# Kernel tuning notes

Hardware: AMD Instinct MI355X
Metric: run time of the kernel (lower is better)

Reference implementation:

```python
import jax, jax.numpy as jnp
import numpy as np

N = 100000
E = 1600000
NFEAT = 128
NHID1 = 128
NHID2 = 128
NCLASS = 40


def setup_inputs() -> dict:
    key = jax.random.key(0)
    ks = jax.random.split(key, 16)
    x = jax.random.normal(ks[0], (N, NFEAT), dtype=jnp.float32)
    src = jax.random.randint(ks[1], (E,), 0, N, dtype=jnp.int32)
    dst = jax.random.randint(ks[2], (E,), 0, N, dtype=jnp.int32)
    s = 0.05
    params = {
        # SAGE layer 1: self branch and neighbor branch
        'w1s': jax.random.normal(ks[3], (NFEAT, NHID1), dtype=jnp.float32) * s,
        'b1s': jnp.zeros((NHID1,), dtype=jnp.float32),
        'w1n': jax.random.normal(ks[4], (NFEAT, NHID1), dtype=jnp.float32) * s,
        'b1n': jnp.zeros((NHID1,), dtype=jnp.float32),
        # SAGE layer 2 (input dim 2*NHID1)
        'w2s': jax.random.normal(ks[5], (2 * NHID1, NHID2), dtype=jnp.float32) * s,
        'b2s': jnp.zeros((NHID2,), dtype=jnp.float32),
        'w2n': jax.random.normal(ks[6], (2 * NHID1, NHID2), dtype=jnp.float32) * s,
        'b2n': jnp.zeros((NHID2,), dtype=jnp.float32),
        # final linear head (input dim 2*NHID2)
        'wfc': jax.random.normal(ks[7], (2 * NHID2, NCLASS), dtype=jnp.float32) * s,
        'bfc': jnp.zeros((NCLASS,), dtype=jnp.float32),
    }
    return {'x': x, 'src': src, 'dst': dst, **params}


def _neigh_mean(h, src, dst, n_nodes):
    # mean aggregation == spmm(row-normalized adj, h), via segment sum over edges
    msg = jax.ops.segment_sum(h[src], dst, num_segments=n_nodes)  # [N, d]
    cnt = jax.ops.segment_sum(jnp.ones((src.shape[0],), h.dtype), dst, num_segments=n_nodes)
    return msg / jnp.maximum(cnt, 1.0)[:, None]


def _sage_layer(h, src, dst, ws, bs, wn, bn):
    neigh = _neigh_mean(h, src, dst, h.shape[0])
    return jnp.concatenate([h @ ws + bs, neigh @ wn + bn], axis=1)


def _l2_normalize(h, eps=1e-12):
    nrm = jnp.sqrt(jnp.sum(h * h, axis=1, keepdims=True))
    return h / jnp.maximum(nrm, eps)


def reference(x, src, dst, w1s, b1s, w1n, b1n, w2s, b2s, w2n, b2n, wfc, bfc):
    h = jax.nn.relu(_sage_layer(x, src, dst, w1s, b1s, w1n, b1n))  # [N, 2*NHID1]
    h = _l2_normalize(h)
    # dropout is identity in eval mode
    h = jax.nn.relu(_sage_layer(h, src, dst, w2s, b2s, w2n, b2n))  # [N, 2*NHID2]
    h = _l2_normalize(h)
    return h @ wfc + bfc  # [N, NCLASS]
```

## Files before the change

### kernel.cpp

```cpp
#include <hip/hip_runtime.h>
#include <hip/hip_bf16.h>


#define N_NODES 100000
#define N_EDGES 1600000
#define NBUCK   196
#define BCAP    12288
#define PB_CAP  14336
#define CHUNK   4096

typedef unsigned short u16;
typedef unsigned int u32;
typedef __bf16 bf16x8 __attribute__((ext_vector_type(8)));
typedef float  f32x4  __attribute__((ext_vector_type(4)));

__device__ __forceinline__ u16 f2b(float f) {
  unsigned x = __builtin_bit_cast(unsigned, f);
  unsigned r = x + 0x7fffu + ((x >> 16) & 1u);
  return (u16)(r >> 16);
}
__device__ __forceinline__ bf16x8 ldfrag(const u16* p) {
  uint4 u = *reinterpret_cast<const uint4*>(p);
  return __builtin_bit_cast(bf16x8, u);
}
__device__ __forceinline__ void unpack8(uint4 u, float* f) {
  f[0] = __builtin_bit_cast(float, u.x << 16);
  f[1] = __builtin_bit_cast(float, u.x & 0xffff0000u);
  f[2] = __builtin_bit_cast(float, u.y << 16);
  f[3] = __builtin_bit_cast(float, u.y & 0xffff0000u);
  f[4] = __builtin_bit_cast(float, u.z << 16);
  f[5] = __builtin_bit_cast(float, u.z & 0xffff0000u);
  f[6] = __builtin_bit_cast(float, u.w << 16);
  f[7] = __builtin_bit_cast(float, u.w & 0xffff0000u);
}
__device__ __forceinline__ uint4 pack8(const float* f) {
  uint4 u;
  u.x = (u32)f2b(f[0]) | ((u32)f2b(f[1]) << 16);
  u.y = (u32)f2b(f[2]) | ((u32)f2b(f[3]) << 16);
  u.z = (u32)f2b(f[4]) | ((u32)f2b(f[5]) << 16);
  u.w = (u32)f2b(f[6]) | ((u32)f2b(f[7]) << 16);
  return u;
}

__global__ __launch_bounds__(256) void prep_weights(
    const float* __restrict__ w1s, const float* __restrict__ w1n,
    const float* __restrict__ w2s, const float* __restrict__ w2n,
    const float* __restrict__ wfc,
    u16* __restrict__ WT1, u16* __restrict__ WT2, u16* __restrict__ WFCT,
    int* __restrict__ cntg, u16* __restrict__ XWn) {
  int i = blockIdx.x * 256 + threadIdx.x;
  if (i < 32768) {
    int c = i >> 7, k = i & 127;
    float v = (c < 128) ? w1s[k * 128 + c] : w1n[k * 128 + (c - 128)];
    WT1[c * 128 + k] = f2b(v);
  } else if (i < 32768 + 65536) {
    int j = i - 32768;
    int c = j >> 8, k = j & 255;
    float v = (c < 128) ? w2s[k * 128 + c] : w2n[k * 128 + (c - 128)];
    WT2[c * 256 + k] = f2b(v);
  } else if (i < 98304 + 12288) {
    int j = i - 98304;
    int c = j >> 8, k = j & 255;
    float v = (c < 40) ? wfc[k * 40 + c] : 0.f;
    WFCT[c * 256 + k] = f2b(v);
  } else {
    int t = threadIdx.x;
    if (t < NBUCK) cntg[t] = 0;
    if (t >= 128 && t < 256) XWn[(size_t)N_NODES * 128 + (t - 128)] = 0;
  }
}

__device__ __forceinline__ int wave_incl_scan(int x, int lane) {
#pragma unroll
  for (int d = 1; d < 64; d <<= 1) {
    int n = __shfl_up(x, d, 64);
    if (lane >= d) x += n;
  }
  return x;
}

__global__ __launch_bounds__(256) void bucket_kernel(
    const int* __restrict__ src, const int* __restrict__ dst,
    int* __restrict__ cntg, u32* __restrict__ pairBuf) {
  __shared__ unsigned hist[NBUCK];
  __shared__ unsigned gbase[NBUCK];
  __shared__ int sws[4];
  __shared__ u32 stage[CHUNK];
  __shared__ int tgt[CHUNK];
  const int tid = threadIdx.x, lane = tid & 63, wid = tid >> 6;
  const int e0 = blockIdx.x * CHUNK;

  for (int i = tid; i < NBUCK; i += 256) hist[i] = 0u;
  __syncthreads();

  u32 myW[16];
  int myR[16], myB[16];
#pragma unroll
  for (int k = 0; k < 16; ++k) {
    int e = e0 + k * 256 + tid;
    if (e < N_EDGES) {
      unsigned d = (unsigned)dst[e];
      myW[k] = ((d & 511u) << 17) | (unsigned)src[e];
      myB[k] = (int)(d >> 9);
      myR[k] = (int)atomicAdd(&hist[myB[k]], 1u);
    } else {
      myB[k] = -1;
    }
  }
  __syncthreads();

  int cnt = (tid < NBUCK) ? (int)hist[tid] : 0;
  int inc = wave_incl_scan(cnt, lane);
  if (lane == 63) sws[wid] = inc;
  __syncthreads();
  if (wid == 0) {
    int s = (lane < 4) ? sws[lane] : 0;
    s = wave_incl_scan(s, lane);
    if (lane < 4) sws[lane] = s;
  }
  __syncthreads();
  int excl = (wid ? sws[wid - 1] : 0) + inc - cnt;
  int gofs = 0;
  if (tid < NBUCK && cnt > 0) gofs = tid * BCAP + atomicAdd(&cntg[tid], cnt);
  __syncthreads();
  if (tid < NBUCK) {
    hist[tid] = (unsigned)excl;
    gbase[tid] = (unsigned)gofs;
  }
  __syncthreads();

#pragma unroll
  for (int k = 0; k < 16; ++k) {
    if (myB[k] >= 0) {
      int slot = (int)hist[myB[k]] + myR[k];
      stage[slot] = myW[k];
      tgt[slot] = (int)gbase[myB[k]] + myR[k];
    }
  }
  __syncthreads();
  int nvalid = N_EDGES - e0;
  if (nvalid > CHUNK) nvalid = CHUNK;
  for (int i = tid; i < nvalid; i += 256) pairBuf[tgt[i]] = stage[i];
}

__global__ __launch_bounds__(512) void csr_build(
    const u32* __restrict__ pairBuf, const int* __restrict__ cntg,
    int* __restrict__ rowptr, int* __restrict__ degA, int* __restrict__ csr) {
  __shared__ int lcnt[512];
  __shared__ int lofs[512];
  __shared__ int sws[8];
  __shared__ int cstage[PB_CAP];
  const int b = blockIdx.x, tid = threadIdx.x;
  const int lane = tid & 63, wid = tid >> 6;
  int nb = cntg[b];
  if (nb > BCAP) nb = BCAP;
  const u32* pp = pairBuf + (size_t)b * BCAP;

  lcnt[tid] = 0;
  __syncthreads();
  for (int i = tid; i < nb; i += 512) atomicAdd(&lcnt[(pp[i] >> 17) & 511], 1);
  __syncthreads();
  int dg = lcnt[tid];
  int pd = (dg + 7) & ~7;
  int inc = wave_incl_scan(pd, lane);
  if (lane == 63) sws[wid] = inc;
  __syncthreads();
  if (wid == 0) {
    int s = (lane < 8) ? sws[lane] : 0;
    s = wave_incl_scan(s, lane);
    if (lane < 8) sws[lane] = s;
  }
  __syncthreads();
  int excl = (wid ? sws[wid - 1] : 0) + inc - pd;
  int ptot = sws[7];
  int node = b * 512 + tid;
  if (node < N_NODES) {
    rowptr[node] = b * PB_CAP + excl;
    degA[node] = dg;
  }
  lofs[tid] = excl;
  __syncthreads();
  for (int i = tid; i < nb; i += 512) {
    u32 pr = pp[i];
    int pos = atomicAdd(&lofs[(pr >> 17) & 511], 1);
    if (pos < PB_CAP) cstage[pos] = (int)(pr & 0x1FFFFu);
  }
  __syncthreads();
  for (int k = excl + dg; k < excl + pd; ++k)
    if (k < PB_CAP) cstage[k] = N_NODES;
  __syncthreads();
  if (ptot > PB_CAP) ptot = PB_CAP;
  for (int i = tid; i < ptot; i += 512) csr[b * PB_CAP + i] = cstage[i];
}

__device__ __forceinline__ void agg_node(
    const u16* __restrict__ Xs, const u16* __restrict__ Xn,
    const int* __restrict__ rowptr, const int* __restrict__ degA,
    const int* __restrict__ csr, const float* __restrict__ bs,
    const float* __restrict__ bn, int node, int g, int lc,
    float* sf, float* nf) {
  int beg = rowptr[node], dg = degA[node];
  int cnt = (dg + 7) & ~7;
  float acc[8] = {0.f, 0.f, 0.f, 0.f, 0.f, 0.f, 0.f, 0.f};
  const u16* colbase = Xn + lc * 8;
  const int* cp = csr + beg;
  for (int j = 0; j < cnt; j += 8) {
    int s0 = cp[j + g];
    int s1 = cp[j + 4 + g];
    uint4 u0 = *reinterpret_cast<const uint4*>(colbase + (size_t)s0 * 128);
    uint4 u1 = *reinterpret_cast<const uint4*>(colbase + (size_t)s1 * 128);
    float f0[8], f1[8];
    unpack8(u0, f0);
    unpack8(u1, f1);
#pragma unroll
    for (int i = 0; i < 8; ++i) acc[i] += f0[i] + f1[i];
  }
#pragma unroll
  for (int i = 0; i < 8; ++i) {
    acc[i] += __shfl_xor(acc[i], 32, 64);
    acc[i] += __shfl_xor(acc[i], 16, 64);
  }
  float inv = 1.f / (float)(dg > 0 ? dg : 1);
  uint4 sv4 = *reinterpret_cast<const uint4*>(Xs + (size_t)node * 128 + lc * 8);
  unpack8(sv4, sf);
  float4 b0 = *reinterpret_cast<const float4*>(bs + lc * 8);
  float4 b1 = *reinterpret_cast<const float4*>(bs + lc * 8 + 4);
  float4 c0 = *reinterpret_cast<const float4*>(bn + lc * 8);
  float4 c1 = *reinterpret_cast<const float4*>(bn + lc * 8 + 4);
  float bsv[8] = {b0.x, b0.y, b0.z, b0.w, b1.x, b1.y, b1.z, b1.w};
  float bnv[8] = {c0.x, c0.y, c0.z, c0.w, c1.x, c1.y, c1.z, c1.w};
  float ss = 0.f;
#pragma unroll
  for (int i = 0; i < 8; ++i) {
    sf[i] = fmaxf(sf[i] + bsv[i], 0.f);
    nf[i] = fmaxf(acc[i] * inv + bnv[i], 0.f);
    ss += sf[i] * sf[i] + nf[i] * nf[i];
  }
  ss += __shfl_xor(ss, 1, 64);
  ss += __shfl_xor(ss, 2, 64);
  ss += __shfl_xor(ss, 4, 64);
  ss += __shfl_xor(ss, 8, 64);
  float sc = 1.f / fmaxf(sqrtf(ss), 1e-12f);
#pragma unroll
  for (int i = 0; i < 8; ++i) {
    sf[i] *= sc;
    nf[i] *= sc;
  }
}

__global__ __launch_bounds__(256) void agg_epi_kernel(
    const u16* __restrict__ Xs, const u16* __restrict__ Xn,
    const int* __restrict__ rowptr, const int* __restrict__ degA,
    const int* __restrict__ csr, const float* __restrict__ bs,
    const float* __restrict__ bn, u16* __restrict__ H) {
  int node = (int)((blockIdx.x * 256 + threadIdx.x) >> 6);
  int lane = threadIdx.x & 63;
  if (node >= N_NODES) return;
  const int g = lane >> 4, lc = lane & 15;
  float sf[8], nf[8];
  agg_node(Xs, Xn, rowptr, degA, csr, bs, bn, node, g, lc, sf, nf);
  if (g == 0) {
    *reinterpret_cast<uint4*>(H + (size_t)node * 256 + lc * 8) = pack8(sf);
  } else if (g == 1) {
    *reinterpret_cast<uint4*>(H + (size_t)node * 256 + 128 + lc * 8) = pack8(nf);
  }
}

__global__ __launch_bounds__(512) void agg_fc_kernel(
    const u16* __restrict__ Xs, const u16* __restrict__ Xn,
    const int* __restrict__ rowptr, const int* __restrict__ degA,
    const int* __restrict__ csr, const float* __restrict__ bs,
    const float* __restrict__ bn, const u16* __restrict__ WFCT,
    const float* __restrict__ bfc, float* __restrict__ Out) {
  __shared__ u16 hh[32][264];
  __shared__ u16 wf[48][264];
  const int tid = threadIdx.x, w = tid >> 6, lane = tid & 63;
  const int g = lane >> 4, lc = lane & 15;
  const int nb0 = blockIdx.x * 32;

  for (int i = tid; i < 1536; i += 512) {
    int row = i >> 5, col = (i & 31) * 8;
    *reinterpret_cast<uint4*>(&wf[row][col]) =
        *reinterpret_cast<const uint4*>(WFCT + row * 256 + col);
  }

  for (int t = 0; t < 4; ++t) {
    int r = w * 4 + t;
    int node = nb0 + r;
    if (node < N_NODES) {
      float sf[8], nf[8];
      agg_node(Xs, Xn, rowptr, degA, csr, bs, bn, node, g, lc, sf, nf);
      if (g == 0) {
        *reinterpret_cast<uint4*>(&hh[r][lc * 8]) = pack8(sf);
      } else if (g == 1) {
        *reinterpret_cast<uint4*>(&hh[r][128 + lc * 8]) = pack8(nf);
      }
    } else {
      uint4 z = {0u, 0u, 0u, 0u};
      if (g == 0) *reinterpret_cast<uint4*>(&hh[r][lc * 8]) = z;
      else if (g == 1) *reinterpret_cast<uint4*>(&hh[r][128 + lc * 8]) = z;
    }
  }
  __syncthreads();

  const int rt = w & 1, cg = w >> 1;
  if (cg < 3) {
    const int lrow = lane & 15, lk = lane >> 4;
    f32x4 acc = {0.f, 0.f, 0.f, 0.f};
#pragma unroll
    for (int ks = 0; ks < 8; ++ks) {
      bf16x8 a = ldfrag(&hh[rt * 16 + lrow][ks * 32 + lk * 8]);
      bf16x8 b = ldfrag(&wf[cg * 16 + lrow][ks * 32 + lk * 8]);
      acc = __builtin_amdgcn_mfma_f32_16x16x32_bf16(a, b, acc, 0, 0, 0);
    }
#pragma unroll
    for (int j = 0; j < 4; ++j) {
      int row = nb0 + rt * 16 + lk * 4 + j;
      int col = cg * 16 + lrow;
      if (row < N_NODES && col < 40) Out[(size_t)row * 40 + col] = acc[j] + bfc[col];
    }
  }
}

__global__ __launch_bounds__(512) void gemm1_kernel(
    const float* __restrict__ A, const u16* __restrict__ WT,
    u16* __restrict__ Cs, u16* __restrict__ Cn) {
  __shared__ u16 lb[256 * 128];
  char* lbc = reinterpret_cast<char*>(lb);
  const int tid = threadIdx.x;
  for (int i = tid; i < 4096; i += 512) {
    uint4 v = *reinterpret_cast<const uint4*>(WT + i * 8);
    int byte = i * 16;
    int swz = byte ^ (((byte >> 8) & 7) << 4);
    *reinterpret_cast<uint4*>(lbc + swz) = v;
  }

  const int w = tid >> 6, lane = tid & 63;
  const int lrow = lane & 15, lk = lane >> 4;
  const int xr = (lrow & 7) << 4;
  const int rbase = blockIdx.x * 128 + w * 16;

  bf16x8 af[4];
  {
    int r = rbase + lrow;
    if (r >= N_NODES) r = N_NODES - 1;
    const float* ap = A + (size_t)r * 128 + lk * 8;
#pragma unroll
    for (int ks = 0; ks < 4; ++ks) {
      float4 f0 = *reinterpret_cast<const float4*>(ap + ks * 32);
      float4 f1 = *reinterpret_cast<const float4*>(ap + ks * 32 + 4);
      float f[8] = {f0.x, f0.y, f0.z, f0.w, f1.x, f1.y, f1.z, f1.w};
      af[ks] = __builtin_bit_cast(bf16x8, pack8(f));
    }
  }
  __syncthreads();

  f32x4 acc[16];
#pragma unroll
  for (int ct = 0; ct < 16; ++ct) acc[ct] = f32x4{0.f, 0.f, 0.f, 0.f};
#pragma unroll
  for (int ks = 0; ks < 4; ++ks) {
#pragma unroll
    for (int ct = 0; ct < 16; ++ct) {
      int byte = (ct * 16 + lrow) * 256 + ks * 64 + lk * 16;
      bf16x8 b = __builtin_bit_cast(
          bf16x8, *reinterpret_cast<const uint4*>(lbc + (byte ^ xr)));
      acc[ct] = __builtin_amdgcn_mfma_f32_16x16x32_bf16(af[ks], b, acc[ct], 0, 0, 0);
    }
  }
#pragma unroll
  for (int j = 0; j < 4; ++j) {
    int r = rbase + lk * 4 + j;
    if (r < N_NODES) {
      u16* cs = Cs + (size_t)r * 128 + lrow;
      u16* cn = Cn + (size_t)r * 128 + lrow;
#pragma unroll
      for (int ct = 0; ct < 8; ++ct) cs[ct * 16] = f2b(acc[ct][j]);
#pragma unroll
      for (int ct = 0; ct < 8; ++ct) cn[ct * 16] = f2b(acc[8 + ct][j]);
    }
  }
}

__global__ __launch_bounds__(512) void gemm2_kernel(
    const u16* __restrict__ A, const u16* __restrict__ WT,
    u16* __restrict__ Cs, u16* __restrict__ Cn) {
  __shared__ u16 lb[128 * 256];
  char* lbc = reinterpret_cast<char*>(lb);
  const int tid = threadIdx.x;
  const int w = tid >> 6, lane = tid & 63;
  const int lrow = lane & 15, lk = lane >> 4;
  const int xr = (lrow & 7) << 4;
  const int rbase = blockIdx.x * 128 + w * 16;

  bf16x8 af[8];
  {
    int r = rbase + lrow;
    if (r >= N_NODES) r = N_NODES - 1;
    const u16* ap = A + (size_t)r * 256 + lk * 8;
#pragma unroll
    for (int ks = 0; ks < 8; ++ks) af[ks] = ldfrag(ap + ks * 32);
  }

#pragma unroll
  for (int half = 0; half < 2; ++half) {
    const u16* Wsrc = WT + (size_t)half * 128 * 256;
    for (int i = tid; i < 4096; i += 512) {
      uint4 v = *reinterpret_cast<const uint4*>(Wsrc + i * 8);
      int byte = i * 16;
      int swz = byte ^ (((byte >> 9) & 7) << 4);
      *reinterpret_cast<uint4*>(lbc + swz) = v;
    }
    __syncthreads();

    f32x4 acc[8];
#pragma unroll
    for (int ct = 0; ct < 8; ++ct) acc[ct] = f32x4{0.f, 0.f, 0.f, 0.f};
#pragma unroll
    for (int ks = 0; ks < 8; ++ks) {
#pragma unroll
      for (int ct = 0; ct < 8; ++ct) {
        int byte = (ct * 16 + lrow) * 512 + ks * 64 + lk * 16;
        bf16x8 b = __builtin_bit_cast(
            bf16x8, *reinterpret_cast<const uint4*>(lbc + (byte ^ xr)));
        acc[ct] = __builtin_amdgcn_mfma_f32_16x16x32_bf16(af[ks], b, acc[ct], 0, 0, 0);
      }
    }
    u16* __restrict__ Cout = half ? Cn : Cs;
#pragma unroll
    for (int j = 0; j < 4; ++j) {
      int r = rbase + lk * 4 + j;
      if (r < N_NODES) {
        u16* cp = Cout + (size_t)r * 128 + lrow;
#pragma unroll
        for (int ct = 0; ct < 8; ++ct) cp[ct * 16] = f2b(acc[ct][j]);
      }
    }
    __syncthreads();
  }
}

extern "C" void kernel_launch(void* const* d_in, const int* in_sizes, int n_in,
                              void* d_out, int out_size, void* d_ws, size_t ws_size,
                              hipStream_t stream) {
  const float* x = (const float*)d_in[0];
  const int* src = (const int*)d_in[1];
  const int* dst = (const int*)d_in[2];
  const float* w1s = (const float*)d_in[3];
  const float* b1s = (const float*)d_in[4];
  const float* w1n = (const float*)d_in[5];
  const float* b1n = (const float*)d_in[6];
  const float* w2s = (const float*)d_in[7];
  const float* b2s = (const float*)d_in[8];
  const float* w2n = (const float*)d_in[9];
  const float* b2n = (const float*)d_in[10];
  const float* wfc = (const float*)d_in[11];
  const float* bfc = (const float*)d_in[12];
  float* out = (float*)d_out;

  char* p = (char*)d_ws;
  auto alloc = [&](size_t bytes) {
    char* r = p;
    p += (bytes + 255) & ~(size_t)255;
    return r;
  };
  u16* XWs = (u16*)alloc((size_t)N_NODES * 128 * 2);
  u16* XWn = (u16*)alloc(((size_t)N_NODES + 1) * 128 * 2);
  u16* h1 = (u16*)alloc((size_t)N_NODES * 256 * 2);
  u16* WT1 = (u16*)alloc(32768 * 2);
  u16* WT2 = (u16*)alloc(65536 * 2);
  u16* WFCT = (u16*)alloc(12288 * 2);
  u32* pairBuf = (u32*)alloc((size_t)NBUCK * BCAP * 4);
  int* cntg = (int*)alloc(NBUCK * 4);
  int* rowptr = (int*)alloc((size_t)N_NODES * 4);
  int* degA = (int*)alloc((size_t)N_NODES * 4);
  int* csr = (int*)alloc((size_t)NBUCK * PB_CAP * 4);

  prep_weights<<<433, 256, 0, stream>>>(w1s, w1n, w2s, w2n, wfc, WT1, WT2, WFCT,
                                        cntg, XWn);
  bucket_kernel<<<391, 256, 0, stream>>>(src, dst, cntg, pairBuf);
  csr_build<<<NBUCK, 512, 0, stream>>>(pairBuf, cntg, rowptr, degA, csr);

  gemm1_kernel<<<782, 512, 0, stream>>>(x, WT1, XWs, XWn);
  agg_epi_kernel<<<25000, 256, 0, stream>>>(XWs, XWn, rowptr, degA, csr, b1s, b1n, h1);
  gemm2_kernel<<<782, 512, 0, stream>>>(h1, WT2, XWs, XWn);
  agg_fc_kernel<<<3125, 512, 0, stream>>>(XWs, XWn, rowptr, degA, csr, b2s, b2n,
                                          WFCT, bfc, out);
}
```

Baseline: 359.9 us.

## Merge setup kernels, co-schedule CSR build with GEMM1, persistent layer-1 aggregation

Weight prep and edge bucketing become one launch, split by block index. CSR construction and the first GEMM share a second launch, split the same way, using 64KB of dynamic shared memory. This cuts kernel launches and lets the two independent stages overlap on the device. The bucket-counter and pad-row zeroing move to hipMemsetAsync calls. The layer-1 aggregation becomes a grid-stride loop over 2048 blocks. The final aggregation+FC kernel now uses an XOR-swizzled LDS tile and reads the FC weights straight from global memory instead of staging them.

```diff
diff --git a/kernel.cpp b/kernel.cpp
--- a/kernel.cpp
+++ b/kernel.cpp
@@ -8,6 +8,8 @@
 #define BCAP    12288
 #define PB_CAP  14336
 #define CHUNK   4096
+#define PREP_BLKS 432
+#define GEMM1_BLKS 782
 
 typedef unsigned short u16;
 typedef unsigned int u32;
@@ -42,13 +44,22 @@
   return u;
 }
 
-__global__ __launch_bounds__(256) void prep_weights(
-    const float* __restrict__ w1s, const float* __restrict__ w1n,
-    const float* __restrict__ w2s, const float* __restrict__ w2n,
-    const float* __restrict__ wfc,
-    u16* __restrict__ WT1, u16* __restrict__ WT2, u16* __restrict__ WFCT,
-    int* __restrict__ cntg, u16* __restrict__ XWn) {
-  int i = blockIdx.x * 256 + threadIdx.x;
+__device__ __forceinline__ int wave_incl_scan(int x, int lane) {
+#pragma unroll
+  for (int d = 1; d < 64; d <<= 1) {
+    int n = __shfl_up(x, d, 64);
+    if (lane >= d) x += n;
+  }
+  return x;
+}
+
+__device__ void prep_body(int bid, const float* __restrict__ w1s,
+                          const float* __restrict__ w1n,
+                          const float* __restrict__ w2s,
+                          const float* __restrict__ w2n,
+                          const float* __restrict__ wfc, u16* __restrict__ WT1,
+                          u16* __restrict__ WT2, u16* __restrict__ WFCT) {
+  int i = bid * 256 + threadIdx.x;
   if (i < 32768) {
     int c = i >> 7, k = i & 127;
     float v = (c < 128) ? w1s[k * 128 + c] : w1n[k * 128 + (c - 128)];
@@ -58,37 +69,32 @@
     int c = j >> 8, k = j & 255;
     float v = (c < 128) ? w2s[k * 128 + c] : w2n[k * 128 + (c - 128)];
     WT2[c * 256 + k] = f2b(v);
-  } else if (i < 98304 + 12288) {
+  } else {
     int j = i - 98304;
     int c = j >> 8, k = j & 255;
     float v = (c < 40) ? wfc[k * 40 + c] : 0.f;
     WFCT[c * 256 + k] = f2b(v);
-  } else {
-    int t = threadIdx.x;
-    if (t < NBUCK) cntg[t] = 0;
-    if (t >= 128 && t < 256) XWn[(size_t)N_NODES * 128 + (t - 128)] = 0;
-  }
-}
-
-__device__ __forceinline__ int wave_incl_scan(int x, int lane) {
-#pragma unroll
-  for (int d = 1; d < 64; d <<= 1) {
-    int n = __shfl_up(x, d, 64);
-    if (lane >= d) x += n;
-  }
-  return x;
-}
-
-__global__ __launch_bounds__(256) void bucket_kernel(
+  }
+}
+
+__global__ __launch_bounds__(256) void prep_bucket_kernel(
+    const float* __restrict__ w1s, const float* __restrict__ w1n,
+    const float* __restrict__ w2s, const float* __restrict__ w2n,
+    const float* __restrict__ wfc, u16* __restrict__ WT1,
+    u16* __restrict__ WT2, u16* __restrict__ WFCT,
     const int* __restrict__ src, const int* __restrict__ dst,
     int* __restrict__ cntg, u32* __restrict__ pairBuf) {
+  if (blockIdx.x < PREP_BLKS) {
+    prep_body(blockIdx.x, w1s, w1n, w2s, w2n, wfc, WT1, WT2, WFCT);
+    return;
+  }
   __shared__ unsigned hist[NBUCK];
   __shared__ unsigned gbase[NBUCK];
   __shared__ int sws[4];
   __shared__ u32 stage[CHUNK];
   __shared__ int tgt[CHUNK];
   const int tid = threadIdx.x, lane = tid & 63, wid = tid >> 6;
-  const int e0 = blockIdx.x * CHUNK;
+  const int e0 = (blockIdx.x - PREP_BLKS) * CHUNK;
 
   for (int i = tid; i < NBUCK; i += 256) hist[i] = 0u;
   __syncthreads();
@@ -143,14 +149,14 @@
   for (int i = tid; i < nvalid; i += 256) pairBuf[tgt[i]] = stage[i];
 }
 
-__global__ __launch_bounds__(512) void csr_build(
-    const u32* __restrict__ pairBuf, const int* __restrict__ cntg,
-    int* __restrict__ rowptr, int* __restrict__ degA, int* __restrict__ csr) {
-  __shared__ int lcnt[512];
-  __shared__ int lofs[512];
-  __shared__ int sws[8];
-  __shared__ int cstage[PB_CAP];
-  const int b = blockIdx.x, tid = threadIdx.x;
+__device__ void csr_body(char* smem, int b, const u32* __restrict__ pairBuf,
+                         const int* __restrict__ cntg, int* __restrict__ rowptr,
+                         int* __restrict__ degA, int* __restrict__ csr) {
+  int* lcnt = (int*)smem;
+  int* lofs = lcnt + 512;
+  int* sws = lofs + 512;
+  int* cstage = sws + 8;
+  const int tid = threadIdx.x;
   const int lane = tid & 63, wid = tid >> 6;
   int nb = cntg[b];
   if (nb > BCAP) nb = BCAP;
@@ -191,6 +197,79 @@
   __syncthreads();
   if (ptot > PB_CAP) ptot = PB_CAP;
   for (int i = tid; i < ptot; i += 512) csr[b * PB_CAP + i] = cstage[i];
+}
+
+__device__ void gemm1_body(char* smem, int bid, const float* __restrict__ A,
+                           const u16* __restrict__ WT, u16* __restrict__ Cs,
+                           u16* __restrict__ Cn) {
+  u16* lb = (u16*)smem;
+  char* lbc = smem;
+  const int tid = threadIdx.x;
+  for (int i = tid; i < 4096; i += 512) {
+    uint4 v = *reinterpret_cast<const uint4*>(WT + i * 8);
+    int byte = i * 16;
+    int swz = byte ^ (((byte >> 8) & 7) << 4);
+    *reinterpret_cast<uint4*>(lbc + swz) = v;
+  }
+
+  const int w = tid >> 6, lane = tid & 63;
+  const int lrow = lane & 15, lk = lane >> 4;
+  const int xr = (lrow & 7) << 4;
+  const int rbase = bid * 128 + w * 16;
+
+  bf16x8 af[4];
+  {
+    int r = rbase + lrow;
+    if (r >= N_NODES) r = N_NODES - 1;
+    const float* ap = A + (size_t)r * 128 + lk * 8;
+#pragma unroll
+    for (int ks = 0; ks < 4; ++ks) {
+      float4 f0 = *reinterpret_cast<const float4*>(ap + ks * 32);
+      float4 f1 = *reinterpret_cast<const float4*>(ap + ks * 32 + 4);
+      float f[8] = {f0.x, f0.y, f0.z, f0.w, f1.x, f1.y, f1.z, f1.w};
+      af[ks] = __builtin_bit_cast(bf16x8, pack8(f));
+    }
+  }
+  __syncthreads();
+
+  f32x4 acc[16];
+#pragma unroll
+  for (int ct = 0; ct < 16; ++ct) acc[ct] = f32x4{0.f, 0.f, 0.f, 0.f};
+#pragma unroll
+  for (int ks = 0; ks < 4; ++ks) {
+#pragma unroll
+    for (int ct = 0; ct < 16; ++ct) {
+      int byte = (ct * 16 + lrow) * 256 + ks * 64 + lk * 16;
+      bf16x8 b = __builtin_bit_cast(
+          bf16x8, *reinterpret_cast<const uint4*>(lbc + (byte ^ xr)));
+      acc[ct] = __builtin_amdgcn_mfma_f32_16x16x32_bf16(af[ks], b, acc[ct], 0, 0, 0);
+    }
+  }
+#pragma unroll
+  for (int j = 0; j < 4; ++j) {
+    int r = rbase + lk * 4 + j;
+    if (r < N_NODES) {
+      u16* cs = Cs + (size_t)r * 128 + lrow;
+      u16* cn = Cn + (size_t)r * 128 + lrow;
+#pragma unroll
+      for (int ct = 0; ct < 8; ++ct) cs[ct * 16] = f2b(acc[ct][j]);
+#pragma unroll
+      for (int ct = 0; ct < 8; ++ct) cn[ct * 16] = f2b(acc[8 + ct][j]);
+    }
+  }
+}
+
+__global__ __launch_bounds__(512) void csr_gemm1_kernel(
+    const u32* __restrict__ pairBuf, const int* __restrict__ cntg,
+    int* __restrict__ rowptr, int* __restrict__ degA, int* __restrict__ csr,
+    const float* __restrict__ A, const u16* __restrict__ WT,
+    u16* __restrict__ Cs, u16* __restrict__ Cn) {
+  extern __shared__ char smem[];
+  if (blockIdx.x < NBUCK) {
+    csr_body(smem, blockIdx.x, pairBuf, cntg, rowptr, degA, csr);
+  } else {
+    gemm1_body(smem, blockIdx.x - NBUCK, A, WT, Cs, Cn);
+  }
 }
 
 __device__ __forceinline__ void agg_node(
@@ -253,131 +332,17 @@
     const int* __restrict__ rowptr, const int* __restrict__ degA,
     const int* __restrict__ csr, const float* __restrict__ bs,
     const float* __restrict__ bn, u16* __restrict__ H) {
-  int node = (int)((blockIdx.x * 256 + threadIdx.x) >> 6);
-  int lane = threadIdx.x & 63;
-  if (node >= N_NODES) return;
+  const int lane = threadIdx.x & 63;
   const int g = lane >> 4, lc = lane & 15;
-  float sf[8], nf[8];
-  agg_node(Xs, Xn, rowptr, degA, csr, bs, bn, node, g, lc, sf, nf);
-  if (g == 0) {
-    *reinterpret_cast<uint4*>(H + (size_t)node * 256 + lc * 8) = pack8(sf);
-  } else if (g == 1) {
-    *reinterpret_cast<uint4*>(H + (size_t)node * 256 + 128 + lc * 8) = pack8(nf);
-  }
-}
-
-__global__ __launch_bounds__(512) void agg_fc_kernel(
-    const u16* __restrict__ Xs, const u16* __restrict__ Xn,
-    const int* __restrict__ rowptr, const int* __restrict__ degA,
-    const int* __restrict__ csr, const float* __restrict__ bs,
-    const float* __restrict__ bn, const u16* __restrict__ WFCT,
-    const float* __restrict__ bfc, float* __restrict__ Out) {
-  __shared__ u16 hh[32][264];
-  __shared__ u16 wf[48][264];
-  const int tid = threadIdx.x, w = tid >> 6, lane = tid & 63;
-  const int g = lane >> 4, lc = lane & 15;
-  const int nb0 = blockIdx.x * 32;
-
-  for (int i = tid; i < 1536; i += 512) {
-    int row = i >> 5, col = (i & 31) * 8;
-    *reinterpret_cast<uint4*>(&wf[row][col]) =
-        *reinterpret_cast<const uint4*>(WFCT + row * 256 + col);
-  }
-
-  for (int t = 0; t < 4; ++t) {
-    int r = w * 4 + t;
-    int node = nb0 + r;
-    if (node < N_NODES) {
-      float sf[8], nf[8];
-      agg_node(Xs, Xn, rowptr, degA, csr, bs, bn, node, g, lc, sf, nf);
-      if (g == 0) {
-        *reinterpret_cast<uint4*>(&hh[r][lc * 8]) = pack8(sf);
-      } else if (g == 1) {
-        *reinterpret_cast<uint4*>(&hh[r][128 + lc * 8]) = pack8(nf);
-      }
-    } else {
-      uint4 z = {0u, 0u, 0u, 0u};
-      if (g == 0) *reinterpret_cast<uint4*>(&hh[r][lc * 8]) = z;
-      else if (g == 1) *reinterpret_cast<uint4*>(&hh[r][128 + lc * 8]) = z;
-    }
-  }
-  __syncthreads();
-
-  const int rt = w & 1, cg = w >> 1;
-  if (cg < 3) {
-    const int lrow = lane & 15, lk = lane >> 4;
-    f32x4 acc = {0.f, 0.f, 0.f, 0.f};
-#pragma unroll
-    for (int ks = 0; ks < 8; ++ks) {
-      bf16x8 a = ldfrag(&hh[rt * 16 + lrow][ks * 32 + lk * 8]);
-      bf16x8 b = ldfrag(&wf[cg * 16 + lrow][ks * 32 + lk * 8]);
-      acc = __builtin_amdgcn_mfma_f32_16x16x32_bf16(a, b, acc, 0, 0, 0);
-    }
-#pragma unroll
-    for (int j = 0; j < 4; ++j) {
-      int row = nb0 + rt * 16 + lk * 4 + j;
-      int col = cg * 16 + lrow;
-      if (row < N_NODES && col < 40) Out[(size_t)row * 40 + col] = acc[j] + bfc[col];
-    }
-  }
-}
-
-__global__ __launch_bounds__(512) void gemm1_kernel(
-    const float* __restrict__ A, const u16* __restrict__ WT,
-    u16* __restrict__ Cs, u16* __restrict__ Cn) {
-  __shared__ u16 lb[256 * 128];
-  char* lbc = reinterpret_cast<char*>(lb);
-  const int tid = threadIdx.x;
-  for (int i = tid; i < 4096; i += 512) {
-    uint4 v = *reinterpret_cast<const uint4*>(WT + i * 8);
-    int byte = i * 16;
-    int swz = byte ^ (((byte >> 8) & 7) << 4);
-    *reinterpret_cast<uint4*>(lbc + swz) = v;
-  }
-
-  const int w = tid >> 6, lane = tid & 63;
-  const int lrow = lane & 15, lk = lane >> 4;
-  const int xr = (lrow & 7) << 4;
-  const int rbase = blockIdx.x * 128 + w * 16;
-
-  bf16x8 af[4];
-  {
-    int r = rbase + lrow;
-    if (r >= N_NODES) r = N_NODES - 1;
-    const float* ap = A + (size_t)r * 128 + lk * 8;
-#pragma unroll
-    for (int ks = 0; ks < 4; ++ks) {
-      float4 f0 = *reinterpret_cast<const float4*>(ap + ks * 32);
-      float4 f1 = *reinterpret_cast<const float4*>(ap + ks * 32 + 4);
-      float f[8] = {f0.x, f0.y, f0.z, f0.w, f1.x, f1.y, f1.z, f1.w};
-      af[ks] = __builtin_bit_cast(bf16x8, pack8(f));
-    }
-  }
-  __syncthreads();
-
-  f32x4 acc[16];
-#pragma unroll
-  for (int ct = 0; ct < 16; ++ct) acc[ct] = f32x4{0.f, 0.f, 0.f, 0.f};
-#pragma unroll
-  for (int ks = 0; ks < 4; ++ks) {
-#pragma unroll
-    for (int ct = 0; ct < 16; ++ct) {
-      int byte = (ct * 16 + lrow) * 256 + ks * 64 + lk * 16;
-      bf16x8 b = __builtin_bit_cast(
-          bf16x8, *reinterpret_cast<const uint4*>(lbc + (byte ^ xr)));
-      acc[ct] = __builtin_amdgcn_mfma_f32_16x16x32_bf16(af[ks], b, acc[ct], 0, 0, 0);
-    }
-  }
-#pragma unroll
-  for (int j = 0; j < 4; ++j) {
-    int r = rbase + lk * 4 + j;
-    if (r < N_NODES) {
-      u16* cs = Cs + (size_t)r * 128 + lrow;
-      u16* cn = Cn + (size_t)r * 128 + lrow;
-#pragma unroll
-      for (int ct = 0; ct < 8; ++ct) cs[ct * 16] = f2b(acc[ct][j]);
-#pragma unroll
-      for (int ct = 0; ct < 8; ++ct) cn[ct * 16] = f2b(acc[8 + ct][j]);
+  const int wave0 = blockIdx.x * 4 + (threadIdx.x >> 6);
+  const int stride = gridDim.x * 4;
+  for (int node = wave0; node < N_NODES; node += stride) {
+    float sf[8], nf[8];
+    agg_node(Xs, Xn, rowptr, degA, csr, bs, bn, node, g, lc, sf, nf);
+    if (g == 0) {
+      *reinterpret_cast<uint4*>(H + (size_t)node * 256 + lc * 8) = pack8(sf);
+    } else if (g == 1) {
+      *reinterpret_cast<uint4*>(H + (size_t)node * 256 + 128 + lc * 8) = pack8(nf);
     }
   }
 }
@@ -437,6 +402,64 @@
       }
     }
     __syncthreads();
+  }
+}
+
+__global__ __launch_bounds__(512) void agg_fc_kernel(
+    const u16* __restrict__ Xs, const u16* __restrict__ Xn,
+    const int* __restrict__ rowptr, const int* __restrict__ degA,
+    const int* __restrict__ csr, const float* __restrict__ bs,
+    const float* __restrict__ bn, const u16* __restrict__ WFCT,
+    const float* __restrict__ bfc, float* __restrict__ Out) {
+  __shared__ u16 hh[32 * 256];
+  char* hhb = reinterpret_cast<char*>(hh);
+  const int tid = threadIdx.x, w = tid >> 6, lane = tid & 63;
+  const int g = lane >> 4, lc = lane & 15;
+  const int nb0 = blockIdx.x * 32;
+
+  for (int t = 0; t < 4; ++t) {
+    int r = w * 4 + t;
+    int node = nb0 + r;
+    int xr_r = (r & 7) << 4;
+    uint4 val;
+    int cbyte;
+    if (node < N_NODES) {
+      float sf[8], nf[8];
+      agg_node(Xs, Xn, rowptr, degA, csr, bs, bn, node, g, lc, sf, nf);
+      val = (g == 0) ? pack8(sf) : pack8(nf);
+    } else {
+      val = uint4{0u, 0u, 0u, 0u};
+    }
+    if (g == 0) {
+      cbyte = (lc * 16) ^ xr_r;
+      *reinterpret_cast<uint4*>(hhb + r * 512 + cbyte) = val;
+    } else if (g == 1) {
+      cbyte = 256 + ((lc * 16) ^ xr_r);
+      *reinterpret_cast<uint4*>(hhb + r * 512 + cbyte) = val;
+    }
+  }
+  __syncthreads();
+
+  const int rt = w & 1, cg = w >> 1;
+  if (cg < 3) {
+    const int lrow = lane & 15, lk = lane >> 4;
+    const int arow = rt * 16 + lrow;
+    const int xr_a = (arow & 7) << 4;
+    f32x4 acc = {0.f, 0.f, 0.f, 0.f};
+#pragma unroll
+    for (int ks = 0; ks < 8; ++ks) {
+      int cbyte = (ks * 64 + lk * 16) ^ xr_a;
+      bf16x8 a = __builtin_bit_cast(
+          bf16x8, *reinterpret_cast<const uint4*>(hhb + arow * 512 + cbyte));
+      bf16x8 b = ldfrag(WFCT + (size_t)(cg * 16 + lrow) * 256 + ks * 32 + lk * 8);
+      acc = __builtin_amdgcn_mfma_f32_16x16x32_bf16(a, b, acc, 0, 0, 0);
+    }
+#pragma unroll
+    for (int j = 0; j < 4; ++j) {
+      int row = nb0 + rt * 16 + lk * 4 + j;
+      int col = cg * 16 + lrow;
+      if (row < N_NODES && col < 40) Out[(size_t)row * 40 + col] = acc[j] + bfc[col];
+    }
   }
 }
 
@@ -476,14 +499,15 @@
   int* degA = (int*)alloc((size_t)N_NODES * 4);
   int* csr = (int*)alloc((size_t)NBUCK * PB_CAP * 4);
 
-  prep_weights<<<433, 256, 0, stream>>>(w1s, w1n, w2s, w2n, wfc, WT1, WT2, WFCT,
-                                        cntg, XWn);
-  bucket_kernel<<<391, 256, 0, stream>>>(src, dst, cntg, pairBuf);
-  csr_build<<<NBUCK, 512, 0, stream>>>(pairBuf, cntg, rowptr, degA, csr);
-
-  gemm1_kernel<<<782, 512, 0, stream>>>(x, WT1, XWs, XWn);
-  agg_epi_kernel<<<25000, 256, 0, stream>>>(XWs, XWn, rowptr, degA, csr, b1s, b1n, h1);
-  gemm2_kernel<<<782, 512, 0, stream>>>(h1, WT2, XWs, XWn);
+  hipMemsetAsync(cntg, 0, NBUCK * 4, stream);
+  hipMemsetAsync(XWn + (size_t)N_NODES * 128, 0, 256, stream);
+
+  prep_bucket_kernel<<<PREP_BLKS + 391, 256, 0, stream>>>(
+      w1s, w1n, w2s, w2n, wfc, WT1, WT2, WFCT, src, dst, cntg, pairBuf);
+  csr_gemm1_kernel<<<NBUCK + GEMM1_BLKS, 512, 65536, stream>>>(
+      pairBuf, cntg, rowptr, degA, csr, x, WT1, XWs, XWn);
+  agg_epi_kernel<<<2048, 256, 0, stream>>>(XWs, XWn, rowptr, degA, csr, b1s, b1n, h1);
+  gemm2_kernel<<<GEMM1_BLKS, 512, 0, stream>>>(h1, WT2, XWs, XWn);
   agg_fc_kernel<<<3125, 512, 0, stream>>>(XWs, XWn, rowptr, degA, csr, b2s, b2n,
                                           WFCT, bfc, out);
 }
```

Result: no change. 360.9 us (+0.3%).
